# Optimization experiments

Hardware: AMD Instinct MI355X
Metric: run time of the kernel (lower is better)

## Reference

```python
import jax, jax.numpy as jnp
import numpy as np

EPS = 1e-5
RADIUS = 3.0
NSAMPLE = 32


def _bn(x, g, b, axes):
    # BatchNorm (training-mode batch statistics) over given axes; channel is axis 1.
    m = jnp.mean(x, axis=axes, keepdims=True)
    v = jnp.var(x, axis=axes, keepdims=True)
    shape = [1, -1] + [1] * (x.ndim - 2)
    return (x - m) / jnp.sqrt(v + EPS) * g.reshape(shape) + b.reshape(shape)


def _ball_query(xyz, new_xyz, radius, nsample):
    # xyz: (B,N,3) support points, new_xyz: (B,M,3) query points -> idx (B,M,nsample) int32
    # Matches pointnet2 ball_query: first `nsample` points within radius (in index order),
    # padded with the first found index (0 if none found).
    d2 = (jnp.sum(new_xyz ** 2, -1)[:, :, None]
          + jnp.sum(xyz ** 2, -1)[:, None, :]
          - 2.0 * jnp.einsum('bmd,bnd->bmn', new_xyz, xyz))  # (B,M,N)
    mask = d2 < radius * radius
    N = xyz.shape[1]
    scores = jnp.where(mask, -jnp.arange(N, dtype=d2.dtype), -jnp.inf)
    vals, _ = jax.lax.top_k(scores, nsample)  # largest scores = smallest indices, in order
    valid = jnp.isfinite(vals)
    idx = jnp.where(valid, -vals, 0.0).astype(jnp.int32)
    first = idx[..., 0:1]
    return jnp.where(valid, idx, first)


def setup_inputs() -> dict:
    key = jax.random.key(0)
    ks = jax.random.split(key, 8)
    B, N, M, C = 4, 16384, 2048, 128
    inp = {
        'ffps_xyz': jax.random.normal(ks[0], (B, M, 3), jnp.float32),
        'backbone_xyz': jax.random.normal(ks[1], (B, N, 3), jnp.float32),
        'backbone_features': jax.random.normal(ks[2], (B, C, N), jnp.float32),
        'shift_w0': jax.random.normal(ks[3], (64, 3), jnp.float32) * 0.1,
        'shift_g0': jnp.ones((64,), jnp.float32),
        'shift_b0': jnp.zeros((64,), jnp.float32),
        'shift_w1': jax.random.normal(ks[4], (3, 64), jnp.float32) * 0.1,
        'shift_g1': jnp.ones((3,), jnp.float32),
        'shift_b1': jnp.zeros((3,), jnp.float32),
        'mlp_w0': jax.random.normal(ks[5], (128, 131), jnp.float32) * 0.05,
        'mlp_g0': jnp.ones((128,), jnp.float32),
        'mlp_b0': jnp.zeros((128,), jnp.float32),
        'mlp_w1': jax.random.normal(ks[6], (256, 128), jnp.float32) * 0.05,
        'mlp_g1': jnp.ones((256,), jnp.float32),
        'mlp_b1': jnp.zeros((256,), jnp.float32),
    }
    return inp


def reference(ffps_xyz, backbone_xyz, backbone_features,
              shift_w0, shift_g0, shift_b0, shift_w1, shift_g1, shift_b1,
              mlp_w0, mlp_g0, mlp_b0, mlp_w1, mlp_g1, mlp_b1):
    # shift_layer: Conv1d(1x1)+BN1d+ReLU stack on candidate coordinates
    q = ffps_xyz.transpose(0, 2, 1)  # (B,3,M)
    h = jax.nn.relu(_bn(jnp.einsum('oc,bcm->bom', shift_w0, q), shift_g0, shift_b0, (0, 2)))
    h = jax.nn.relu(_bn(jnp.einsum('oc,bcm->bom', shift_w1, h), shift_g1, shift_b1, (0, 2)))
    new_xyz = h.transpose(0, 2, 1)  # (B,M,3) shifted candidate centers

    # QueryAndGroup(use_xyz=True)
    idx = _ball_query(backbone_xyz, new_xyz, RADIUS, NSAMPLE)        # (B,M,K)
    grouped_xyz = jax.vmap(lambda x, i: x[i])(backbone_xyz, idx)      # (B,M,K,3)
    grouped_feat = jax.vmap(lambda f, i: f[:, i])(backbone_features, idx)  # (B,C,M,K)
    rel = (grouped_xyz - new_xyz[:, :, None, :]).transpose(0, 3, 1, 2)     # (B,3,M,K)
    g = jnp.concatenate([rel, grouped_feat], axis=1)                  # (B,3+C,M,K)

    # Conv2d(1x1)+BN2d+ReLU stack
    g = jax.nn.relu(_bn(jnp.einsum('oc,bcmk->bomk', mlp_w0, g), mlp_g0, mlp_b0, (0, 2, 3)))
    g = jax.nn.relu(_bn(jnp.einsum('oc,bcmk->bomk', mlp_w1, g), mlp_g1, mlp_b1, (0, 2, 3)))

    # max-pool over neighbor dim, squeeze, transpose -> (B,M,C_out)
    out = jnp.max(g, axis=3)  # (B,C_out,M)
    return out.transpose(0, 2, 1)
```

## Files before the change

kernel.cpp:

```cpp
#include <hip/hip_runtime.h>
#include <cstddef>
#include <cstdint>

#define B_ 4
#define N_ 16384
#define M_ 2048
#define C_ 128
#define NQ (B_*M_)
#define NSAMP 32
#define SAMP (NQ*NSAMP)
#define EPS_ 1e-5f
#define R2_ 9.0f

typedef short s8v  __attribute__((ext_vector_type(8)));
typedef short s4v  __attribute__((ext_vector_type(4)));
typedef float f32x4 __attribute__((ext_vector_type(4)));

#define ST_COPIES 8
#define ST_S0S 0
#define ST_S0Q 64
#define ST_S1S 128
#define ST_S1Q 136
#define ST_M1S 144
#define ST_M1Q 272
#define ST_M2S 400
#define ST_M2Q 656

__device__ __forceinline__ unsigned short f2bf(float f) {
    unsigned int u = __builtin_bit_cast(unsigned int, f);
    u += 0x7fffu + ((u >> 16) & 1u);
    return (unsigned short)(u >> 16);
}
__device__ __forceinline__ float bf2f(unsigned short h) {
    unsigned int u = ((unsigned int)h) << 16;
    return __builtin_bit_cast(float, u);
}

__global__ void k_prep_w(const float* __restrict__ w0, const float* __restrict__ w1,
                         unsigned short* __restrict__ w0p, unsigned short* __restrict__ w1p) {
    int i = blockIdx.x * 256 + threadIdx.x;
    const int tot0 = 128 * 160;
    if (i < tot0) {
        int o = i / 160, c = i - o * 160;
        float v = 0.f;
        if (c < 128)      v = w0[o * 131 + 3 + c];
        else if (c < 131) v = w0[o * 131 + (c - 128)];
        w0p[i] = f2bf(v);
    }
    int j = i - tot0;
    if (j >= 0 && j < 256 * 128) w1p[j] = f2bf(w1[j]);
}

__global__ void k_transpose(const float* __restrict__ feat, unsigned short* __restrict__ featT) {
    __shared__ unsigned short tl[64][130];
    int b  = blockIdx.x >> 8;
    int n0 = (blockIdx.x & 255) * 64;
    const float* src = feat + (size_t)b * C_ * N_;
    int t = threadIdx.x;
    for (int i = 0; i < 32; ++i) {
        int lin = i * 256 + t;
        int c = lin >> 6, n = lin & 63;
        tl[n][c] = f2bf(src[(size_t)c * N_ + n0 + n]);
    }
    __syncthreads();
    unsigned short* dst = featT + ((size_t)b * N_ + n0) * 128;
    #pragma unroll
    for (int i = 0; i < 4; ++i) {
        int lin = i * 256 + t;
        int n = lin >> 4, cg = lin & 15;
        s8v v;
        #pragma unroll
        for (int e = 0; e < 8; ++e) v[e] = (short)tl[n][cg*8 + e];
        *(s8v*)(dst + (size_t)n * 128 + cg * 8) = v;
    }
}

__global__ void k_shift0(const float* __restrict__ xyz, const float* __restrict__ w0s,
                         float* __restrict__ t0, float* __restrict__ stats) {
    __shared__ float w[192];
    __shared__ float ps[4][64], pq[4][64];
    int t = threadIdx.x, wave = t >> 6, lane = t & 63;
    if (t < 192) w[t] = w0s[t];
    __syncthreads();
    int p = blockIdx.x * 256 + t;
    float q0 = xyz[p*3], q1 = xyz[p*3+1], q2 = xyz[p*3+2];
    float* orow = t0 + (size_t)p * 64;
    #pragma unroll
    for (int o = 0; o < 64; ++o) {
        float v = w[3*o]*q0 + w[3*o+1]*q1 + w[3*o+2]*q2;
        orow[o] = v;
        float s = v, sq = v * v;
        #pragma unroll
        for (int mk = 32; mk; mk >>= 1) { s += __shfl_xor(s, mk); sq += __shfl_xor(sq, mk); }
        if (lane == 0) { ps[wave][o] = s; pq[wave][o] = sq; }
    }
    __syncthreads();
    if (t < 64) {
        float s = ps[0][t] + ps[1][t] + ps[2][t] + ps[3][t];
        float q = pq[0][t] + pq[1][t] + pq[2][t] + pq[3][t];
        atomicAdd(&stats[ST_S0S + t], s);
        atomicAdd(&stats[ST_S0Q + t], q);
    }
}

__global__ void k_shift1(const float* __restrict__ t0, const float* __restrict__ w1s,
                         const float* __restrict__ g0, const float* __restrict__ b0,
                         float* __restrict__ t1, float* __restrict__ stats) {
    __shared__ float aa[64], bb[64], wl[192];
    __shared__ float ps[4][3], pq[4][3];
    int t = threadIdx.x, wave = t >> 6, lane = t & 63;
    if (t < 64) {
        float mean = stats[ST_S0S + t] * (1.f / NQ);
        float var  = stats[ST_S0Q + t] * (1.f / NQ) - mean * mean;
        float a = g0[t] * rsqrtf(var + EPS_);
        aa[t] = a; bb[t] = b0[t] - mean * a;
    }
    if (t < 192) wl[t] = w1s[t];
    __syncthreads();
    int p = blockIdx.x * 256 + t;
    const f32x4* xr = (const f32x4*)(t0 + (size_t)p * 64);
    float v0 = 0.f, v1 = 0.f, v2 = 0.f;
    #pragma unroll
    for (int i = 0; i < 16; ++i) {
        f32x4 x = xr[i];
        #pragma unroll
        for (int j = 0; j < 4; ++j) {
            int c = 4*i + j;
            float h = fmaxf(0.f, aa[c] * x[j] + bb[c]);
            v0 += wl[c] * h; v1 += wl[64 + c] * h; v2 += wl[128 + c] * h;
        }
    }
    t1[p*3] = v0; t1[p*3+1] = v1; t1[p*3+2] = v2;
    float vv[3] = {v0, v1, v2};
    #pragma unroll
    for (int o = 0; o < 3; ++o) {
        float s = vv[o], q = vv[o] * vv[o];
        #pragma unroll
        for (int mk = 32; mk; mk >>= 1) { s += __shfl_xor(s, mk); q += __shfl_xor(q, mk); }
        if (lane == 0) { ps[wave][o] = s; pq[wave][o] = q; }
    }
    __syncthreads();
    if (t < 3) {
        float s = ps[0][t] + ps[1][t] + ps[2][t] + ps[3][t];
        float q = pq[0][t] + pq[1][t] + pq[2][t] + pq[3][t];
        atomicAdd(&stats[ST_S1S + t], s);
        atomicAdd(&stats[ST_S1Q + t], q);
    }
}

__global__ void k_shift2(const float* __restrict__ t1, const float* __restrict__ g1,
                         const float* __restrict__ b1, const float* __restrict__ stats,
                         float* __restrict__ nxyz) {
    int p = blockIdx.x * 256 + threadIdx.x;
    for (int o = 0; o < 3; ++o) {
        float mean = stats[ST_S1S + o] * (1.f / NQ);
        float var  = stats[ST_S1Q + o] * (1.f / NQ) - mean * mean;
        float a = g1[o] * rsqrtf(var + EPS_);
        float bbv = b1[o] - mean * a;
        nxyz[p*3+o] = fmaxf(0.f, a * t1[p*3+o] + bbv);
    }
}

__global__ void k_ballq(const float* __restrict__ bxyz, const float* __restrict__ nxyz,
                        int* __restrict__ idxb) {
    int wq   = blockIdx.x * 4 + (threadIdx.x >> 6);
    int lane = threadIdx.x & 63;
    int b    = wq >> 11;
    float qx = nxyz[wq*3], qy = nxyz[wq*3+1], qz = nxyz[wq*3+2];
    float sq = __fadd_rn(__fadd_rn(__fmul_rn(qx,qx), __fmul_rn(qy,qy)), __fmul_rn(qz,qz));
    const float* bp = bxyz + (size_t)b * N_ * 3;
    int* op = idxb + (size_t)wq * 32;
    unsigned long long below = (lane == 63) ? ~0ull >> 1 : ((1ull << lane) - 1ull);
    int cnt = 0, first = 0;
    for (int j0 = 0; j0 < N_ && cnt < 32; j0 += 512) {
        float xs[8], ys[8], zs[8];
        #pragma unroll
        for (int u = 0; u < 8; ++u) {
            int j = j0 + u*64 + lane;
            xs[u] = bp[j*3]; ys[u] = bp[j*3+1]; zs[u] = bp[j*3+2];
        }
        #pragma unroll
        for (int u = 0; u < 8; ++u) {
            int j = j0 + u*64 + lane;
            float x = xs[u], y = ys[u], z = zs[u];
            float sx  = __fadd_rn(__fadd_rn(__fmul_rn(x,x), __fmul_rn(y,y)), __fmul_rn(z,z));
            float dot = __fadd_rn(__fadd_rn(__fmul_rn(qx,x), __fmul_rn(qy,y)), __fmul_rn(qz,z));
            float d2  = __fsub_rn(__fadd_rn(sq, sx), __fmul_rn(2.0f, dot));
            unsigned long long m = __ballot(d2 < R2_);
            if (cnt == 0 && m != 0ull) first = j0 + u*64 + __ffsll((long long)m) - 1;
            int pre = cnt + __popcll(m & below);
            if (((m >> lane) & 1ull) && pre < 32) op[pre] = j;
            cnt += __popcll(m);
        }
    }
    if (cnt < 32) {
        if (cnt == 0) first = 0;
        for (int k = cnt + lane; k < 32; k += 64) op[k] = first;
    }
}

__global__ void __launch_bounds__(256)
k_gemm1(const unsigned short* __restrict__ featT, const float* __restrict__ bxyz,
        const float* __restrict__ nxyz, const int* __restrict__ idxb,
        const unsigned short* __restrict__ w0p, unsigned short* __restrict__ y1,
        float* __restrict__ stats) {
    __shared__ unsigned short gt[64][168];
    __shared__ int pidx[256];
    __shared__ float nq[8][3];
    int tid  = threadIdx.x;
    int wave = tid >> 6, lane = tid & 63, quad = lane >> 4, l16 = lane & 15;
    int s2 = tid >> 2, part4 = tid & 3;
    int b = blockIdx.x >> 8;
    float* stc = stats + (size_t)(blockIdx.x & (ST_COPIES-1)) * 1024;

    s8v bfr[2][5];
    #pragma unroll
    for (int g = 0; g < 2; ++g)
        #pragma unroll
        for (int kk = 0; kk < 5; ++kk)
            bfr[g][kk] = *(const s8v*)(w0p + (wave*32 + g*16 + l16)*160 + kk*32 + quad*8);

    pidx[tid] = idxb[blockIdx.x * 256 + tid];
    if (tid < 24) nq[tid / 3][tid % 3] = nxyz[blockIdx.x * 24 + tid];
    if (tid < 64)
        for (int c = 131; c < 160; ++c) gt[tid][c] = 0;
    __syncthreads();

    s8v pv[4]; float prel0 = 0.f, prel1 = 0.f, prel2 = 0.f;
    {
        int pp = pidx[s2];
        const unsigned short* src = featT + ((size_t)(b * N_ + pp)) * 128 + part4 * 32;
        pv[0] = *(const s8v*)src;        pv[1] = *(const s8v*)(src + 8);
        pv[2] = *(const s8v*)(src + 16); pv[3] = *(const s8v*)(src + 24);
        if (tid < 64) {
            int pq_ = pidx[tid];
            const float* bx = bxyz + (size_t)(b * N_ + pq_) * 3;
            int q = tid >> 5;
            prel0 = bx[0] - nq[q][0]; prel1 = bx[1] - nq[q][1]; prel2 = bx[2] - nq[q][2];
        }
    }
    float csum[2] = {}, csq[2] = {};

    for (int r = 0; r < 4; ++r) {
        __syncthreads();
        *(s8v*)&gt[s2][part4*32]      = pv[0];
        *(s8v*)&gt[s2][part4*32 + 8]  = pv[1];
        *(s8v*)&gt[s2][part4*32 + 16] = pv[2];
        *(s8v*)&gt[s2][part4*32 + 24] = pv[3];
        if (tid < 64) {
            gt[tid][128] = f2bf(prel0); gt[tid][129] = f2bf(prel1); gt[tid][130] = f2bf(prel2);
        }
        if (r + 1 < 4) {
            int pp = pidx[(r+1)*64 + s2];
            const unsigned short* src = featT + ((size_t)(b * N_ + pp)) * 128 + part4 * 32;
            pv[0] = *(const s8v*)src;        pv[1] = *(const s8v*)(src + 8);
            pv[2] = *(const s8v*)(src + 16); pv[3] = *(const s8v*)(src + 24);
            if (tid < 64) {
                int pq_ = pidx[(r+1)*64 + tid];
                const float* bx = bxyz + (size_t)(b * N_ + pq_) * 3;
                int q = (r+1)*2 + (tid >> 5);
                prel0 = bx[0] - nq[q][0]; prel1 = bx[1] - nq[q][1]; prel2 = bx[2] - nq[q][2];
            }
        }
        __syncthreads();
        f32x4 acc[2][4] = {};
        #pragma unroll
        for (int kk = 0; kk < 5; ++kk) {
            s8v at[4];
            #pragma unroll
            for (int t = 0; t < 4; ++t)
                at[t] = *(const s8v*)&gt[t*16 + l16][kk*32 + quad*8];
            #pragma unroll
            for (int g = 0; g < 2; ++g)
                #pragma unroll
                for (int t = 0; t < 4; ++t)
                    acc[g][t] = __builtin_amdgcn_mfma_f32_16x16x32_bf16(at[t], bfr[g][kk], acc[g][t], 0, 0, 0);
        }
        size_t sbase = (size_t)blockIdx.x * 256 + r * 64;
        #pragma unroll
        for (int g = 0; g < 2; ++g) {
            int ch = wave*32 + g*16 + l16;
            #pragma unroll
            for (int t = 0; t < 4; ++t)
                #pragma unroll
                for (int rr = 0; rr < 4; ++rr) {
                    float v = acc[g][t][rr];
                    y1[(sbase + t*16 + quad*4 + rr) * 128 + ch] = f2bf(v);
                    csum[g] += v; csq[g] += v * v;
                }
        }
    }
    #pragma unroll
    for (int g = 0; g < 2; ++g) {
        float s = csum[g], q = csq[g];
        s += __shfl_xor(s, 16); s += __shfl_xor(s, 32);
        q += __shfl_xor(q, 16); q += __shfl_xor(q, 32);
        if (quad == 0) {
            int ch = wave*32 + g*16 + l16;
            atomicAdd(&stc[ST_M1S + ch], s);
            atomicAdd(&stc[ST_M1Q + ch], q);
        }
    }
}

__global__ void __launch_bounds__(256)
k_gemm2(const unsigned short* __restrict__ y1, const unsigned short* __restrict__ w1p,
        const float* __restrict__ g1m, const float* __restrict__ b1m,
        float* __restrict__ stats, float* __restrict__ mx, float* __restrict__ mn) {
    __shared__ unsigned short ht[256][136];
    __shared__ float a1l[128], b1l[128];
    int tid = threadIdx.x;
    float* stc = stats + (size_t)(blockIdx.x & (ST_COPIES-1)) * 1024;
    if (tid < 128) {
        float ssum = 0.f, ssq = 0.f;
        #pragma unroll
        for (int c8 = 0; c8 < ST_COPIES; ++c8) {
            ssum += stats[c8*1024 + ST_M1S + tid];
            ssq  += stats[c8*1024 + ST_M1Q + tid];
        }
        float mean = ssum * (1.f / SAMP);
        float var  = ssq  * (1.f / SAMP) - mean * mean;
        float a = g1m[tid] * rsqrtf(var + EPS_);
        a1l[tid] = a; b1l[tid] = b1m[tid] - mean * a;
    }
    __syncthreads();
    int wave = tid >> 6, lane = tid & 63, quad = lane >> 4, l16 = lane & 15;
    int s = tid >> 3, part = tid & 7;

    float a1r[16], b1r[16];
    {
        const float* ap = &a1l[part * 16];
        const float* bp = &b1l[part * 16];
        #pragma unroll
        for (int i = 0; i < 16; ++i) { a1r[i] = ap[i]; b1r[i] = bp[i]; }
    }
    s8v bfr[4][4];
    #pragma unroll
    for (int g = 0; g < 4; ++g)
        #pragma unroll
        for (int kk = 0; kk < 4; ++kk)
            bfr[g][kk] = *(const s8v*)(w1p + (wave*64 + g*16 + l16)*128 + kk*32 + quad*8);

    size_t base = (size_t)blockIdx.x * 256;
    s8v rv[8][2];
    #pragma unroll
    for (int q = 0; q < 8; ++q) {
        const unsigned short* src = y1 + (base + q*32 + s) * 128 + part * 16;
        rv[q][0] = *(const s8v*)src; rv[q][1] = *(const s8v*)(src + 8);
    }
    #pragma unroll
    for (int q = 0; q < 8; ++q) {
        s8v o0, o1;
        #pragma unroll
        for (int e = 0; e < 8; ++e) {
            float f0 = bf2f((unsigned short)rv[q][0][e]);
            float f1 = bf2f((unsigned short)rv[q][1][e]);
            o0[e] = (short)f2bf(fmaxf(0.f, a1r[e]     * f0 + b1r[e]));
            o1[e] = (short)f2bf(fmaxf(0.f, a1r[8 + e] * f1 + b1r[8 + e]));
        }
        *(s8v*)&ht[q*32 + s][part*16]     = o0;
        *(s8v*)&ht[q*32 + s][part*16 + 8] = o1;
    }
    __syncthreads();

    float csum[4] = {}, csq[4] = {};
    for (int r = 0; r < 4; ++r) {
        f32x4 acc[4][4] = {};
        #pragma unroll
        for (int kk = 0; kk < 4; ++kk) {
            s8v at[4];
            #pragma unroll
            for (int t = 0; t < 4; ++t)
                at[t] = *(const s8v*)&ht[r*64 + t*16 + l16][kk*32 + quad*8];
            #pragma unroll
            for (int g = 0; g < 4; ++g)
                #pragma unroll
                for (int t = 0; t < 4; ++t)
                    acc[g][t] = __builtin_amdgcn_mfma_f32_16x16x32_bf16(at[t], bfr[g][kk], acc[g][t], 0, 0, 0);
        }
        #pragma unroll
        for (int g = 0; g < 4; ++g) {
            float sacc = 0.f, qacc = 0.f;
            #pragma unroll
            for (int t = 0; t < 4; ++t)
                #pragma unroll
                for (int e = 0; e < 4; ++e) {
                    float v = acc[g][t][e];
                    sacc += v; qacc = __builtin_fmaf(v, v, qacc);
                }
            csum[g] += sacc; csq[g] += qacc;
            #pragma unroll
            for (int qh = 0; qh < 2; ++qh) {
                int gq = blockIdx.x * 8 + r*2 + qh;
                f32x4 v0 = acc[g][2*qh], v1 = acc[g][2*qh + 1];
                float hi = fmaxf(fmaxf(fmaxf(v0[0], v0[1]), fmaxf(v0[2], v0[3])),
                                 fmaxf(fmaxf(v1[0], v1[1]), fmaxf(v1[2], v1[3])));
                float lo = fminf(fminf(fminf(v0[0], v0[1]), fminf(v0[2], v0[3])),
                                 fminf(fminf(v1[0], v1[1]), fminf(v1[2], v1[3])));
                hi = fmaxf(hi, __shfl_xor(hi, 16)); hi = fmaxf(hi, __shfl_xor(hi, 32));
                lo = fminf(lo, __shfl_xor(lo, 16)); lo = fminf(lo, __shfl_xor(lo, 32));
                if (quad == 0) {
                    int c = wave*64 + g*16 + l16;
                    mx[(size_t)gq * 256 + c] = hi;
                    mn[(size_t)gq * 256 + c] = lo;
                }
            }
        }
    }
    #pragma unroll
    for (int g = 0; g < 4; ++g) {
        float sv = csum[g], q = csq[g];
        sv += __shfl_xor(sv, 16); sv += __shfl_xor(sv, 32);
        q  += __shfl_xor(q, 16);  q  += __shfl_xor(q, 32);
        if (quad == 0) {
            int c = wave*64 + g*16 + l16;
            atomicAdd(&stc[ST_M2S + c], sv);
            atomicAdd(&stc[ST_M2Q + c], q);
        }
    }
}

__global__ void k_final(const float* __restrict__ mx, const float* __restrict__ mn,
                        const float* __restrict__ g2m, const float* __restrict__ b2m,
                        const float* __restrict__ stats, float* __restrict__ out) {
    int i = blockIdx.x * 256 + threadIdx.x;
    int c = i & 255;
    float ssum = 0.f, ssq = 0.f;
    #pragma unroll
    for (int c8 = 0; c8 < ST_COPIES; ++c8) {
        ssum += stats[c8*1024 + ST_M2S + c];
        ssq  += stats[c8*1024 + ST_M2Q + c];
    }
    float mean = ssum * (1.f / SAMP);
    float var  = ssq  * (1.f / SAMP) - mean * mean;
    float a = g2m[c] * rsqrtf(var + EPS_);
    float bb = b2m[c] - mean * a;
    float v = (a >= 0.f) ? mx[i] : mn[i];
    out[i] = fmaxf(0.f, a * v + bb);
}

extern "C" void kernel_launch(void* const* d_in, const int* in_sizes, int n_in,
                              void* d_out, int out_size, void* d_ws, size_t ws_size,
                              hipStream_t stream) {
    const float* ffps = (const float*)d_in[0];
    const float* bxyz = (const float*)d_in[1];
    const float* feat = (const float*)d_in[2];
    const float* sw0  = (const float*)d_in[3];
    const float* sg0  = (const float*)d_in[4];
    const float* sb0  = (const float*)d_in[5];
    const float* sw1  = (const float*)d_in[6];
    const float* sg1  = (const float*)d_in[7];
    const float* sb1  = (const float*)d_in[8];
    const float* mw0  = (const float*)d_in[9];
    const float* mg0  = (const float*)d_in[10];
    const float* mb0  = (const float*)d_in[11];
    const float* mw1  = (const float*)d_in[12];
    const float* mg1  = (const float*)d_in[13];
    const float* mb1  = (const float*)d_in[14];
    float* out = (float*)d_out;

    char* ws = (char*)d_ws;
    size_t off = 0;
    auto alloc = [&](size_t bytes) -> void* {
        void* p = ws + off;
        off += (bytes + 255) & ~(size_t)255;
        return p;
    };
    float*          stats = (float*)alloc(ST_COPIES * 1024 * 4);
    float*          t0    = (float*)alloc((size_t)NQ * 64 * 4);
    float*          t1    = (float*)alloc((size_t)NQ * 3 * 4);
    float*          nxyz  = (float*)alloc((size_t)NQ * 3 * 4);
    int*            idxb  = (int*)alloc((size_t)NQ * 32 * 4);
    unsigned short* w0p   = (unsigned short*)alloc(128 * 160 * 2);
    unsigned short* w1p   = (unsigned short*)alloc(256 * 128 * 2);
    unsigned short* featT = (unsigned short*)alloc((size_t)B_ * N_ * 128 * 2);
    unsigned short* y1    = (unsigned short*)alloc((size_t)SAMP * 128 * 2);
    float*          mx    = (float*)alloc((size_t)NQ * 256 * 4);
    float*          mn    = (float*)alloc((size_t)NQ * 256 * 4);
    (void)in_sizes; (void)n_in; (void)out_size; (void)ws_size;

    hipMemsetAsync(stats, 0, ST_COPIES * 1024 * 4, stream);
    k_prep_w   <<<208, 256, 0, stream>>>(mw0, mw1, w0p, w1p);
    k_transpose<<<B_ * 256, 256, 0, stream>>>(feat, featT);
    k_shift0   <<<NQ / 256, 256, 0, stream>>>(ffps, sw0, t0, stats);
    k_shift1   <<<NQ / 256, 256, 0, stream>>>(t0, sw1, sg0, sb0, t1, stats);
    k_shift2   <<<NQ / 256, 256, 0, stream>>>(t1, sg1, sb1, stats, nxyz);
    k_ballq    <<<NQ / 4, 256, 0, stream>>>(bxyz, nxyz, idxb);
    k_gemm1    <<<NQ / 8, 256, 0, stream>>>(featT, bxyz, nxyz, idxb, w0p, y1, stats);
    k_gemm2    <<<NQ / 8, 256, 0, stream>>>(y1, w1p, mg0, mb0, stats, mx, mn);
    k_final    <<<NQ, 256, 0, stream>>>(mx, mn, mg1, mb1, stats, out);
}
```

Before: 248.1 us.

## Stage support points in LDS for batched ball query and hoist BN2 coefficients

Ball query now processes 64 queries per block (16 per wave). Support points are staged into shared memory in 4096-point chunks, so each chunk loaded from global memory is reused across many queries instead of each wave streaming the points itself. This costs per-wave serialization over 16 queries and adds block-wide syncs, and the early exit can no longer skip loading later chunks. Separately, the final BN2 scale and shift are computed once in a tiny kernel rather than re-reduced over 8 stat copies by every thread of k_final.

Result: no change. 250.6 us (+1.0%).

```diff
diff --git a/kernel.cpp b/kernel.cpp
--- a/kernel.cpp
+++ b/kernel.cpp
@@ -161,41 +161,64 @@
     }
 }
 
-__global__ void k_ballq(const float* __restrict__ bxyz, const float* __restrict__ nxyz,
-                        int* __restrict__ idxb) {
-    int wq   = blockIdx.x * 4 + (threadIdx.x >> 6);
-    int lane = threadIdx.x & 63;
-    int b    = wq >> 11;
-    float qx = nxyz[wq*3], qy = nxyz[wq*3+1], qz = nxyz[wq*3+2];
-    float sq = __fadd_rn(__fadd_rn(__fmul_rn(qx,qx), __fmul_rn(qy,qy)), __fmul_rn(qz,qz));
+__global__ void __launch_bounds__(256)
+k_ballq(const float* __restrict__ bxyz, const float* __restrict__ nxyz,
+        int* __restrict__ idxb) {
+    __shared__ float pts[4096 * 3];
+    int tid = threadIdx.x, wave = tid >> 6, lane = tid & 63;
+    int b = blockIdx.x >> 5;
+    int qbase = blockIdx.x * 64 + wave * 16;
     const float* bp = bxyz + (size_t)b * N_ * 3;
-    int* op = idxb + (size_t)wq * 32;
     unsigned long long below = (lane == 63) ? ~0ull >> 1 : ((1ull << lane) - 1ull);
-    int cnt = 0, first = 0;
-    for (int j0 = 0; j0 < N_ && cnt < 32; j0 += 512) {
-        float xs[8], ys[8], zs[8];
-        #pragma unroll
-        for (int u = 0; u < 8; ++u) {
-            int j = j0 + u*64 + lane;
-            xs[u] = bp[j*3]; ys[u] = bp[j*3+1]; zs[u] = bp[j*3+2];
-        }
-        #pragma unroll
-        for (int u = 0; u < 8; ++u) {
-            int j = j0 + u*64 + lane;
-            float x = xs[u], y = ys[u], z = zs[u];
-            float sx  = __fadd_rn(__fadd_rn(__fmul_rn(x,x), __fmul_rn(y,y)), __fmul_rn(z,z));
-            float dot = __fadd_rn(__fadd_rn(__fmul_rn(qx,x), __fmul_rn(qy,y)), __fmul_rn(qz,z));
-            float d2  = __fsub_rn(__fadd_rn(sq, sx), __fmul_rn(2.0f, dot));
-            unsigned long long m = __ballot(d2 < R2_);
-            if (cnt == 0 && m != 0ull) first = j0 + u*64 + __ffsll((long long)m) - 1;
-            int pre = cnt + __popcll(m & below);
-            if (((m >> lane) & 1ull) && pre < 32) op[pre] = j;
-            cnt += __popcll(m);
-        }
-    }
-    if (cnt < 32) {
-        if (cnt == 0) first = 0;
-        for (int k = cnt + lane; k < 32; k += 64) op[k] = first;
+
+    float qx[16], qy[16], qz[16], sq[16];
+    int cnt[16], first[16];
+    #pragma unroll
+    for (int q = 0; q < 16; ++q) {
+        qx[q] = nxyz[(qbase+q)*3]; qy[q] = nxyz[(qbase+q)*3+1]; qz[q] = nxyz[(qbase+q)*3+2];
+        sq[q] = __fadd_rn(__fadd_rn(__fmul_rn(qx[q],qx[q]), __fmul_rn(qy[q],qy[q])), __fmul_rn(qz[q],qz[q]));
+        cnt[q] = 0; first[q] = 0;
+    }
+
+    for (int ch = 0; ch < 4; ++ch) {
+        __syncthreads();
+        {
+            const f32x4* src = (const f32x4*)(bp + ch * 12288);
+            f32x4* d4 = (f32x4*)pts;
+            #pragma unroll
+            for (int i = 0; i < 12; ++i) d4[i*256 + tid] = src[i*256 + tid];
+        }
+        __syncthreads();
+        #pragma unroll
+        for (int q = 0; q < 16; ++q) {
+            if (cnt[q] >= 32) continue;
+            for (int j0 = 0; j0 < 4096 && cnt[q] < 32; j0 += 256) {
+                #pragma unroll
+                for (int u = 0; u < 4; ++u) {
+                    if (cnt[q] < 32) {
+                        int jl = j0 + u*64 + lane;
+                        float x = pts[jl*3], y = pts[jl*3+1], z = pts[jl*3+2];
+                        float sx  = __fadd_rn(__fadd_rn(__fmul_rn(x,x), __fmul_rn(y,y)), __fmul_rn(z,z));
+                        float dot = __fadd_rn(__fadd_rn(__fmul_rn(qx[q],x), __fmul_rn(qy[q],y)), __fmul_rn(qz[q],z));
+                        float d2  = __fsub_rn(__fadd_rn(sq[q], sx), __fmul_rn(2.0f, dot));
+                        unsigned long long m = __ballot(d2 < R2_);
+                        if (cnt[q] == 0 && m != 0ull)
+                            first[q] = ch*4096 + j0 + u*64 + __ffsll((long long)m) - 1;
+                        int pre = cnt[q] + __popcll(m & below);
+                        if (((m >> lane) & 1ull) && pre < 32)
+                            idxb[(size_t)(qbase+q)*32 + pre] = ch*4096 + jl;
+                        cnt[q] += __popcll(m);
+                    }
+                }
+            }
+        }
+    }
+    #pragma unroll
+    for (int q = 0; q < 16; ++q) {
+        if (cnt[q] < 32) {
+            int f = (cnt[q] == 0) ? 0 : first[q];
+            for (int k = cnt[q] + lane; k < 32; k += 64) idxb[(size_t)(qbase+q)*32 + k] = f;
+        }
     }
 }
 
@@ -420,11 +443,9 @@
     }
 }
 
-__global__ void k_final(const float* __restrict__ mx, const float* __restrict__ mn,
-                        const float* __restrict__ g2m, const float* __restrict__ b2m,
-                        const float* __restrict__ stats, float* __restrict__ out) {
-    int i = blockIdx.x * 256 + threadIdx.x;
-    int c = i & 255;
+__global__ void k_bn2(const float* __restrict__ g2m, const float* __restrict__ b2m,
+                      const float* __restrict__ stats, float* __restrict__ ab2) {
+    int c = threadIdx.x;
     float ssum = 0.f, ssq = 0.f;
     #pragma unroll
     for (int c8 = 0; c8 < ST_COPIES; ++c8) {
@@ -434,7 +455,14 @@
     float mean = ssum * (1.f / SAMP);
     float var  = ssq  * (1.f / SAMP) - mean * mean;
     float a = g2m[c] * rsqrtf(var + EPS_);
-    float bb = b2m[c] - mean * a;
+    ab2[c] = a; ab2[256 + c] = b2m[c] - mean * a;
+}
+
+__global__ void k_final(const float* __restrict__ mx, const float* __restrict__ mn,
+                        const float* __restrict__ ab2, float* __restrict__ out) {
+    int i = blockIdx.x * 256 + threadIdx.x;
+    int c = i & 255;
+    float a = ab2[c], bb = ab2[256 + c];
     float v = (a >= 0.f) ? mx[i] : mn[i];
     out[i] = fmaxf(0.f, a * v + bb);
 }
@@ -477,6 +505,7 @@
     unsigned short* y1    = (unsigned short*)alloc((size_t)SAMP * 128 * 2);
     float*          mx    = (float*)alloc((size_t)NQ * 256 * 4);
     float*          mn    = (float*)alloc((size_t)NQ * 256 * 4);
+    float*          ab2   = (float*)alloc(512 * 4);
     (void)in_sizes; (void)n_in; (void)out_size; (void)ws_size;
 
     hipMemsetAsync(stats, 0, ST_COPIES * 1024 * 4, stream);
@@ -485,8 +514,9 @@
     k_shift0   <<<NQ / 256, 256, 0, stream>>>(ffps, sw0, t0, stats);
     k_shift1   <<<NQ / 256, 256, 0, stream>>>(t0, sw1, sg0, sb0, t1, stats);
     k_shift2   <<<NQ / 256, 256, 0, stream>>>(t1, sg1, sb1, stats, nxyz);
-    k_ballq    <<<NQ / 4, 256, 0, stream>>>(bxyz, nxyz, idxb);
+    k_ballq    <<<NQ / 64, 256, 0, stream>>>(bxyz, nxyz, idxb);
     k_gemm1    <<<NQ / 8, 256, 0, stream>>>(featT, bxyz, nxyz, idxb, w0p, y1, stats);
     k_gemm2    <<<NQ / 8, 256, 0, stream>>>(y1, w1p, mg0, mb0, stats, mx, mn);
-    k_final    <<<NQ, 256, 0, stream>>>(mx, mn, mg1, mb1, stats, out);
-}
+    k_bn2      <<<1, 256, 0, stream>>>(mg1, mb1, stats, ab2);
+    k_final    <<<NQ, 256, 0, stream>>>(mx, mn, ab2, out);
+}
```
